# Kernel tuning notes

Measured on AMD Instinct MI355X. Metric: run time of the kernel, lower is better.

## Reference

```python
import jax, jax.numpy as jnp
import numpy as np

D_MODEL = 1024
KEY_MODEL = 1024
D_K = 64
D_V = 64
N_HEAD = 8
PROJ = N_HEAD * D_V  # 512


def setup_inputs() -> dict:
    key = jax.random.key(0)
    ks = jax.random.split(key, 9)
    N, M = 8192, 8192
    s = 0.02
    return {
        "q": jax.random.normal(ks[0], (N, D_MODEL), jnp.float32),
        "k": jax.random.normal(ks[1], (M, KEY_MODEL), jnp.float32),
        "v": jax.random.normal(ks[2], (M, D_MODEL), jnp.float32),
        "Wq": jax.random.normal(ks[3], (D_MODEL, PROJ), jnp.float32) * s,
        "bq": jnp.zeros((PROJ,), jnp.float32),
        "Wk": jax.random.normal(ks[4], (KEY_MODEL, PROJ), jnp.float32) * s,
        "bk": jnp.zeros((PROJ,), jnp.float32),
        "Wv": jax.random.normal(ks[5], (D_MODEL, PROJ), jnp.float32) * s,
        "bv": jnp.zeros((PROJ,), jnp.float32),
    }


def reference(q, k, v, Wq, bq, Wk, bk, Wv, bv):
    # Linear projections (torch nn.Linear: x @ W^T + b; here W stored as [in,out])
    qp = q @ Wq + bq                      # [N, PROJ]
    kp = k @ Wk + bk                      # [M, PROJ]
    vp = v @ Wv + bv                      # [M, PROJ]
    # Note: original scales by d_k (NOT sqrt(d_k)); dropout is identity at eval.
    scores = (qp @ kp.T) / D_K            # [N, M]
    attn = jax.nn.softmax(scores, axis=-1)
    return attn @ vp                      # [N, PROJ]
```

## Files before the change

### kernel.cpp

```cpp
#include <hip/hip_runtime.h>
#include <hip/hip_bf16.h>
#include <stdint.h>
#include <stddef.h>

typedef unsigned short u16;
typedef short bf16x8 __attribute__((ext_vector_type(8)));
typedef short bf16x4 __attribute__((ext_vector_type(4)));
typedef float floatx4 __attribute__((ext_vector_type(4)));

#define N_ROWS 8192
#define D_MODEL 1024
#define PROJ 512
#define MHALF 4096
#define SCALE_LOG2E_DK 0.022542110013890054f

#define VMCNT_WAIT(n) asm volatile("s_waitcnt vmcnt(" #n ")" ::: "memory")

#if __has_builtin(__builtin_amdgcn_exp2f)
#define EXP2(x) __builtin_amdgcn_exp2f(x)
#else
#define EXP2(x) exp2f(x)
#endif

__device__ __forceinline__ float bf2f(u16 u) {
    union { unsigned int i; float f; } x; x.i = ((unsigned int)u) << 16; return x.f;
}
__device__ __forceinline__ u16 f2bf(float f) {
    __hip_bfloat16 h = __float2bfloat16(f);
    return *reinterpret_cast<u16*>(&h);
}

__device__ __forceinline__ void gload_lds16(u16* lds_base, const u16* g) {
    __builtin_amdgcn_global_load_lds(
        (const __attribute__((address_space(1))) void*)g,
        (__attribute__((address_space(3))) void*)lds_base,
        16, 0, 0);
}

__device__ __forceinline__ void stage128x32(u16* lds, const u16* src, int stride,
                                            int wv, int ln) {
    const int rr = ln >> 2;
    const int cc = (ln & 3) << 3;
#pragma unroll
    for (int i = 0; i < 2; ++i) {
        const int rb = i * 64 + wv * 16;
        gload_lds16(lds + rb * 32, src + (size_t)(rb + rr) * stride + cc);
    }
}

__global__ void transpose_w_kernel(const float* __restrict__ in, u16* __restrict__ out,
                                   int R, int C) {
    __shared__ u16 tile[32][33];
    int r = blockIdx.y * 32 + threadIdx.y;
    int c = blockIdx.x * 32 + threadIdx.x;
    tile[threadIdx.y][threadIdx.x] = f2bf(in[(size_t)r * C + c]);
    __syncthreads();
    int ro = blockIdx.x * 32 + threadIdx.y;
    int co = blockIdx.y * 32 + threadIdx.x;
    out[(size_t)ro * R + co] = tile[threadIdx.x][threadIdx.y];
}

__global__ void transpose_kernel(const u16* __restrict__ in, u16* __restrict__ out,
                                 int R, int C) {
    __shared__ u16 tile[32][33];
    int r = blockIdx.y * 32 + threadIdx.y;
    int c = blockIdx.x * 32 + threadIdx.x;
    tile[threadIdx.y][threadIdx.x] = in[(size_t)r * C + c];
    __syncthreads();
    int ro = blockIdx.x * 32 + threadIdx.y;
    int co = blockIdx.y * 32 + threadIdx.x;
    int cp = (co & ~63) | (((co & 15) << 2) + ((co >> 4) & 3));
    out[(size_t)ro * R + cp] = tile[threadIdx.x][threadIdx.y];
}

__global__ __launch_bounds__(256) void convert_bf16_kernel(
    const float* __restrict__ q, const float* __restrict__ k, const float* __restrict__ v,
    u16* __restrict__ qb, u16* __restrict__ kb, u16* __restrict__ vb)
{
    const float* in = (blockIdx.y == 0) ? q : (blockIdx.y == 1) ? k : v;
    u16* out        = (blockIdx.y == 0) ? qb : (blockIdx.y == 1) ? kb : vb;
    size_t i = ((size_t)blockIdx.x * 256 + threadIdx.x) * 8;
    float4 a = *(const float4*)(in + i);
    float4 b = *(const float4*)(in + i + 4);
    bf16x8 o;
    o[0] = (short)f2bf(a.x); o[1] = (short)f2bf(a.y);
    o[2] = (short)f2bf(a.z); o[3] = (short)f2bf(a.w);
    o[4] = (short)f2bf(b.x); o[5] = (short)f2bf(b.y);
    o[6] = (short)f2bf(b.z); o[7] = (short)f2bf(b.w);
    *(bf16x8*)(out + i) = o;
}

__global__ __launch_bounds__(256) void proj_kernel(
    const u16* __restrict__ qb, const u16* __restrict__ kb, const u16* __restrict__ vb,
    const u16* __restrict__ WqT, const u16* __restrict__ WkT, const u16* __restrict__ WvT,
    const float* __restrict__ bq, const float* __restrict__ bk, const float* __restrict__ bv,
    u16* __restrict__ qp, u16* __restrict__ kp, u16* __restrict__ vp)
{
    const int z = blockIdx.z;
    const u16* A      = (z == 0) ? qb  : (z == 1) ? kb  : vb;
    const u16* WT     = (z == 0) ? WqT : (z == 1) ? WkT : WvT;
    const float* bias = (z == 0) ? bq  : (z == 1) ? bk  : bv;
    u16* C            = (z == 0) ? qp  : (z == 1) ? kp  : vp;

    const int m0 = blockIdx.x * 128;
    const int n0 = blockIdx.y * 128;
    __shared__ __align__(16) u16 smem[2 * 128 * 32];
    u16* As = smem;
    u16* Bs = smem + 128 * 32;

    const int t = threadIdx.x;
    const int wv = t >> 6, ln = t & 63;
    const int q16 = ln >> 4, l16 = ln & 15;
    const int wm = (wv & 1) * 64, wn = (wv >> 1) * 64;

    floatx4 acc[4][4] = {};

    for (int k0 = 0; k0 < D_MODEL; k0 += 32) {
        __syncthreads();
        stage128x32(As, A  + (size_t)m0 * D_MODEL + k0, D_MODEL, wv, ln);
        stage128x32(Bs, WT + (size_t)n0 * D_MODEL + k0, D_MODEL, wv, ln);
        __syncthreads();

        bf16x8 af[4], bfr[4];
#pragma unroll
        for (int mi = 0; mi < 4; ++mi)
            af[mi] = *(const bf16x8*)(As + (wm + mi * 16 + l16) * 32 + q16 * 8);
#pragma unroll
        for (int ni = 0; ni < 4; ++ni)
            bfr[ni] = *(const bf16x8*)(Bs + (wn + ni * 16 + l16) * 32 + q16 * 8);
#pragma unroll
        for (int mi = 0; mi < 4; ++mi)
#pragma unroll
            for (int ni = 0; ni < 4; ++ni)
                acc[mi][ni] = __builtin_amdgcn_mfma_f32_16x16x32_bf16(
                    af[mi], bfr[ni], acc[mi][ni], 0, 0, 0);
    }

#pragma unroll
    for (int ni = 0; ni < 4; ++ni) {
        int col = n0 + wn + ni * 16 + l16;
        float bv_ = bias[col];
#pragma unroll
        for (int mi = 0; mi < 4; ++mi)
#pragma unroll
            for (int rr = 0; rr < 4; ++rr) {
                int row = m0 + wm + mi * 16 + q16 * 4 + rr;
                C[(size_t)row * PROJ + col] = f2bf(acc[mi][ni][rr] + bv_);
            }
    }
}

__global__ void zero_l_kernel(float* __restrict__ l) {
    l[blockIdx.x * 256 + threadIdx.x] = 0.f;
}

__global__ __launch_bounds__(256) void score_kernel(
    const u16* __restrict__ qp, const u16* __restrict__ kph,
    u16* __restrict__ P, float* __restrict__ l)
{
    const int m0 = blockIdx.x * 128;
    const int n0 = blockIdx.y * 128;
    __shared__ __align__(16) u16 smem[2 * 128 * 32];
    u16* As = smem;
    u16* Bs = smem + 128 * 32;

    const int t = threadIdx.x;
    const int wv = t >> 6, ln = t & 63;
    const int q16 = ln >> 4, l16 = ln & 15;
    const int wm = (wv & 1) * 64, wn = (wv >> 1) * 64;

    floatx4 acc[4][4] = {};

    for (int k0 = 0; k0 < PROJ; k0 += 32) {
        __syncthreads();
        stage128x32(As, qp  + (size_t)m0 * PROJ + k0, PROJ, wv, ln);
        stage128x32(Bs, kph + (size_t)n0 * PROJ + k0, PROJ, wv, ln);
        __syncthreads();

        bf16x8 af[4], bfr[4];
#pragma unroll
        for (int mi = 0; mi < 4; ++mi)
            af[mi] = *(const bf16x8*)(As + (wm + mi * 16 + l16) * 32 + q16 * 8);
#pragma unroll
        for (int ni = 0; ni < 4; ++ni)
            bfr[ni] = *(const bf16x8*)(Bs + (wn + ni * 16 + l16) * 32 + q16 * 8);
#pragma unroll
        for (int mi = 0; mi < 4; ++mi)
#pragma unroll
            for (int ni = 0; ni < 4; ++ni)
                acc[mi][ni] = __builtin_amdgcn_mfma_f32_16x16x32_bf16(
                    af[mi], bfr[ni], acc[mi][ni], 0, 0, 0);
    }

#pragma unroll
    for (int mi = 0; mi < 4; ++mi)
#pragma unroll
        for (int rr = 0; rr < 4; ++rr) {
            int row = m0 + wm + mi * 16 + q16 * 4 + rr;
            u16* Prow = P + (size_t)row * MHALF + n0 + wn;
            float tot = 0.f;
            bf16x4 pk;
#pragma unroll
            for (int ni = 0; ni < 4; ++ni) {
                float x = acc[mi][ni][rr] * SCALE_LOG2E_DK;
                x = fminf(fmaxf(x, -30.f), 30.f);
                float p = EXP2(x);
                tot += p;
                pk[ni] = (short)f2bf(p);
            }
            *(bf16x4*)(Prow + l16 * 4) = pk;
#pragma unroll
            for (int m = 1; m < 16; m <<= 1)
                tot += __shfl_xor(tot, m, 64);
            if (l16 == 0)
                atomicAdd(&l[row], tot);
        }
}

__global__ __launch_bounds__(256) void pv_kernel(
    const u16* __restrict__ P, const u16* __restrict__ vpTh,
    float* __restrict__ Ofull, u16* __restrict__ Opart, int accum)
{
    const int m0 = blockIdx.x * 128;
    const int n0 = blockIdx.y * 128;
    const int kg = blockIdx.z;
    const int kbase = kg * 2048;
    __shared__ __align__(16) u16 smem[4 * 8192];

    const int t = threadIdx.x;
    const int wv = t >> 6, ln = t & 63;
    const int q16 = ln >> 4, l16 = ln & 15;
    const int wm = (wv & 1) * 64, wn = (wv >> 1) * 64;

    const u16* Abase = P    + (size_t)m0 * MHALF  + kbase;
    const u16* Bbase = vpTh + (size_t)n0 * N_ROWS + kbase;

    floatx4 acc[4][4] = {};

    auto STAGE = [&](int ti) {
        u16* buf = smem + (ti & 3) * 8192;
        stage128x32(buf,        Abase + ti * 32, MHALF,  wv, ln);
        stage128x32(buf + 4096, Bbase + ti * 32, N_ROWS, wv, ln);
    };
    auto COMPUTE = [&](int ti) {
        const u16* As = smem + (ti & 3) * 8192;
        const u16* Bs = As + 4096;
        bf16x8 af[4], bfr[4];
#pragma unroll
        for (int mi = 0; mi < 4; ++mi)
            af[mi] = *(const bf16x8*)(As + (wm + mi * 16 + l16) * 32 + q16 * 8);
#pragma unroll
        for (int ni = 0; ni < 4; ++ni)
            bfr[ni] = *(const bf16x8*)(Bs + (wn + ni * 16 + l16) * 32 + q16 * 8);
#pragma unroll
        for (int mi = 0; mi < 4; ++mi)
#pragma unroll
            for (int ni = 0; ni < 4; ++ni)
                acc[mi][ni] = __builtin_amdgcn_mfma_f32_16x16x32_bf16(
                    af[mi], bfr[ni], acc[mi][ni], 0, 0, 0);
    };

    const int NT = 2048 / 32;
    STAGE(0); STAGE(1); STAGE(2);

    for (int ti = 0; ti < NT - 2; ++ti) {
        VMCNT_WAIT(8);
        __builtin_amdgcn_sched_barrier(0);
        __builtin_amdgcn_s_barrier();
        __builtin_amdgcn_sched_barrier(0);
        if (ti + 3 < NT) STAGE(ti + 3);
        COMPUTE(ti);
    }
    VMCNT_WAIT(4);
    __builtin_amdgcn_sched_barrier(0);
    __builtin_amdgcn_s_barrier();
    __builtin_amdgcn_sched_barrier(0);
    COMPUTE(NT - 2);
    VMCNT_WAIT(0);
    __builtin_amdgcn_sched_barrier(0);
    __builtin_amdgcn_s_barrier();
    __builtin_amdgcn_sched_barrier(0);
    COMPUTE(NT - 1);

#pragma unroll
    for (int ni = 0; ni < 4; ++ni) {
        int col = n0 + wn + ni * 16 + l16;
#pragma unroll
        for (int mi = 0; mi < 4; ++mi)
#pragma unroll
            for (int rr = 0; rr < 4; ++rr) {
                int row = m0 + wm + mi * 16 + q16 * 4 + rr;
                size_t o = (size_t)row * PROJ + col;
                float v = acc[mi][ni][rr];
                if (kg == 0) {
                    if (accum) v += Ofull[o];
                    Ofull[o] = v;
                } else {
                    if (accum) v += bf2f(Opart[o]);
                    Opart[o] = f2bf(v);
                }
            }
    }
}

__global__ void scale_kernel(float* __restrict__ out, const u16* __restrict__ Opart,
                             const float* __restrict__ l)
{
    int idx = blockIdx.x * 256 + threadIdx.x;
    int row = idx >> 9;
    out[idx] = (out[idx] + bf2f(Opart[idx])) / l[row];
}

extern "C" void kernel_launch(void* const* d_in, const int* in_sizes, int n_in,
                              void* d_out, int out_size, void* d_ws, size_t ws_size,
                              hipStream_t stream)
{
    (void)in_sizes; (void)n_in; (void)out_size;
    if (ws_size < ((size_t)101 << 20)) return;

    const float* q  = (const float*)d_in[0];
    const float* k  = (const float*)d_in[1];
    const float* v  = (const float*)d_in[2];
    const float* Wq = (const float*)d_in[3];
    const float* bq = (const float*)d_in[4];
    const float* Wk = (const float*)d_in[5];
    const float* bk = (const float*)d_in[6];
    const float* Wv = (const float*)d_in[7];
    const float* bv = (const float*)d_in[8];

    char* ws = (char*)d_ws;
    u16* qp    = (u16*)(ws);
    u16* kp    = (u16*)(ws + ((size_t)8  << 20));
    u16* vp    = (u16*)(ws + ((size_t)16 << 20));
    u16* vpT   = (u16*)(ws + ((size_t)24 << 20));
    u16* WqT   = (u16*)(ws + ((size_t)32 << 20));
    u16* WkT   = (u16*)(ws + ((size_t)33 << 20));
    u16* WvT   = (u16*)(ws + ((size_t)34 << 20));
    float* l   = (float*)(ws + ((size_t)35 << 20));
    u16* P     = (u16*)(ws + ((size_t)36 << 20));
    u16* qb    = (u16*)(ws + ((size_t)36 << 20));
    u16* kb    = (u16*)(ws + ((size_t)52 << 20));
    u16* vb    = (u16*)(ws + ((size_t)68 << 20));
    u16* Opart = vp;
    float* Ofull = (float*)d_out;

    dim3 tb(32, 32);
    transpose_w_kernel<<<dim3(16, 32), tb, 0, stream>>>(Wq, WqT, 1024, 512);
    transpose_w_kernel<<<dim3(16, 32), tb, 0, stream>>>(Wk, WkT, 1024, 512);
    transpose_w_kernel<<<dim3(16, 32), tb, 0, stream>>>(Wv, WvT, 1024, 512);

    convert_bf16_kernel<<<dim3(4096, 3), 256, 0, stream>>>(q, k, v, qb, kb, vb);

    proj_kernel<<<dim3(64, 4, 3), 256, 0, stream>>>(qb, kb, vb, WqT, WkT, WvT,
                                                    bq, bk, bv, qp, kp, vp);

    transpose_kernel<<<dim3(16, 256), tb, 0, stream>>>(vp, vpT, 8192, 512);

    zero_l_kernel<<<32, 256, 0, stream>>>(l);

    score_kernel<<<dim3(64, 32), 256, 0, stream>>>(qp, kp, P, l);
    pv_kernel<<<dim3(64, 4, 2), 256, 0, stream>>>(P, vpT, Ofull, Opart, 0);
    score_kernel<<<dim3(64, 32), 256, 0, stream>>>(qp, kp + (size_t)MHALF * PROJ, P, l);
    pv_kernel<<<dim3(64, 4, 2), 256, 0, stream>>>(P, vpT + MHALF, Ofull, Opart, 1);

    scale_kernel<<<16384, 256, 0, stream>>>(Ofull, Opart, l);
}
```

Measured before the change: 396.0 us.

## Halve N tile to 64 and double grid for proj and pv kernels

Shrinks the output tile of the projection and PV GEMMs from 128x128 to 128x64, which doubles the number of workgroups so more CUs have work on the 256-CU device. It also swizzles the block-to-tile mapping across XCDs for better L2 locality. The projection kernel moves from a single-buffered, two-barrier loop to the same 4-stage global_load_lds pipeline used in PV. The trade-off is more re-reading of the A operand and lower MFMA arithmetic intensity per block.

```diff
diff --git a/kernel.cpp b/kernel.cpp
--- a/kernel.cpp
+++ b/kernel.cpp
@@ -46,6 +46,14 @@
         const int rb = i * 64 + wv * 16;
         gload_lds16(lds + rb * 32, src + (size_t)(rb + rr) * stride + cc);
     }
+}
+
+__device__ __forceinline__ void stage64x32(u16* lds, const u16* src, int stride,
+                                           int wv, int ln) {
+    const int rr = ln >> 2;
+    const int cc = (ln & 3) << 3;
+    const int rb = wv * 16;
+    gload_lds16(lds + rb * 32, src + (size_t)(rb + rr) * stride + cc);
 }
 
 __global__ void transpose_w_kernel(const float* __restrict__ in, u16* __restrict__ out,
@@ -96,48 +104,75 @@
     const float* __restrict__ bq, const float* __restrict__ bk, const float* __restrict__ bv,
     u16* __restrict__ qp, u16* __restrict__ kp, u16* __restrict__ vp)
 {
-    const int z = blockIdx.z;
+    int orig = blockIdx.x + 64 * (blockIdx.y + 8 * blockIdx.z);
+    int logical = (orig & 7) * 192 + (orig >> 3);
+    const int m0 = (logical & 63) * 128;
+    const int n0 = ((logical >> 6) & 7) * 64;
+    const int z  = logical >> 9;
+
     const u16* A      = (z == 0) ? qb  : (z == 1) ? kb  : vb;
     const u16* WT     = (z == 0) ? WqT : (z == 1) ? WkT : WvT;
     const float* bias = (z == 0) ? bq  : (z == 1) ? bk  : bv;
     u16* C            = (z == 0) ? qp  : (z == 1) ? kp  : vp;
 
-    const int m0 = blockIdx.x * 128;
-    const int n0 = blockIdx.y * 128;
-    __shared__ __align__(16) u16 smem[2 * 128 * 32];
-    u16* As = smem;
-    u16* Bs = smem + 128 * 32;
+    __shared__ __align__(16) u16 smem[4 * 6144];
 
     const int t = threadIdx.x;
     const int wv = t >> 6, ln = t & 63;
     const int q16 = ln >> 4, l16 = ln & 15;
-    const int wm = (wv & 1) * 64, wn = (wv >> 1) * 64;
-
-    floatx4 acc[4][4] = {};
-
-    for (int k0 = 0; k0 < D_MODEL; k0 += 32) {
-        __syncthreads();
-        stage128x32(As, A  + (size_t)m0 * D_MODEL + k0, D_MODEL, wv, ln);
-        stage128x32(Bs, WT + (size_t)n0 * D_MODEL + k0, D_MODEL, wv, ln);
-        __syncthreads();
-
-        bf16x8 af[4], bfr[4];
+    const int wm = (wv & 1) * 64, wn = (wv >> 1) * 32;
+
+    const u16* Abase = A  + (size_t)m0 * D_MODEL;
+    const u16* Bbase = WT + (size_t)n0 * D_MODEL;
+
+    floatx4 acc[4][2] = {};
+
+    auto STAGE = [&](int ti) {
+        u16* buf = smem + (ti & 3) * 6144;
+        stage128x32(buf,        Abase + ti * 32, D_MODEL, wv, ln);
+        stage64x32 (buf + 4096, Bbase + ti * 32, D_MODEL, wv, ln);
+    };
+    auto COMPUTE = [&](int ti) {
+        const u16* As = smem + (ti & 3) * 6144;
+        const u16* Bs = As + 4096;
+        bf16x8 af[4], bfr[2];
 #pragma unroll
         for (int mi = 0; mi < 4; ++mi)
             af[mi] = *(const bf16x8*)(As + (wm + mi * 16 + l16) * 32 + q16 * 8);
 #pragma unroll
-        for (int ni = 0; ni < 4; ++ni)
+        for (int ni = 0; ni < 2; ++ni)
             bfr[ni] = *(const bf16x8*)(Bs + (wn + ni * 16 + l16) * 32 + q16 * 8);
 #pragma unroll
         for (int mi = 0; mi < 4; ++mi)
 #pragma unroll
-            for (int ni = 0; ni < 4; ++ni)
+            for (int ni = 0; ni < 2; ++ni)
                 acc[mi][ni] = __builtin_amdgcn_mfma_f32_16x16x32_bf16(
                     af[mi], bfr[ni], acc[mi][ni], 0, 0, 0);
-    }
-
-#pragma unroll
-    for (int ni = 0; ni < 4; ++ni) {
+    };
+
+    const int NT = D_MODEL / 32;
+    STAGE(0); STAGE(1); STAGE(2);
+    for (int ti = 0; ti < NT - 2; ++ti) {
+        VMCNT_WAIT(6);
+        __builtin_amdgcn_sched_barrier(0);
+        __builtin_amdgcn_s_barrier();
+        __builtin_amdgcn_sched_barrier(0);
+        if (ti + 3 < NT) STAGE(ti + 3);
+        COMPUTE(ti);
+    }
+    VMCNT_WAIT(3);
+    __builtin_amdgcn_sched_barrier(0);
+    __builtin_amdgcn_s_barrier();
+    __builtin_amdgcn_sched_barrier(0);
+    COMPUTE(NT - 2);
+    VMCNT_WAIT(0);
+    __builtin_amdgcn_sched_barrier(0);
+    __builtin_amdgcn_s_barrier();
+    __builtin_amdgcn_sched_barrier(0);
+    COMPUTE(NT - 1);
+
+#pragma unroll
+    for (int ni = 0; ni < 2; ++ni) {
         int col = n0 + wn + ni * 16 + l16;
         float bv_ = bias[col];
 #pragma unroll
@@ -221,41 +256,43 @@
     const u16* __restrict__ P, const u16* __restrict__ vpTh,
     float* __restrict__ Ofull, u16* __restrict__ Opart, int accum)
 {
-    const int m0 = blockIdx.x * 128;
-    const int n0 = blockIdx.y * 128;
-    const int kg = blockIdx.z;
+    int orig = blockIdx.x + 64 * (blockIdx.y + 8 * blockIdx.z);
+    int logical = (orig & 7) * 128 + (orig >> 3);
+    const int m0 = (logical & 63) * 128;
+    const int n0 = ((logical >> 6) & 7) * 64;
+    const int kg = logical >> 9;
     const int kbase = kg * 2048;
-    __shared__ __align__(16) u16 smem[4 * 8192];
+    __shared__ __align__(16) u16 smem[4 * 6144];
 
     const int t = threadIdx.x;
     const int wv = t >> 6, ln = t & 63;
     const int q16 = ln >> 4, l16 = ln & 15;
-    const int wm = (wv & 1) * 64, wn = (wv >> 1) * 64;
+    const int wm = (wv & 1) * 64, wn = (wv >> 1) * 32;
 
     const u16* Abase = P    + (size_t)m0 * MHALF  + kbase;
     const u16* Bbase = vpTh + (size_t)n0 * N_ROWS + kbase;
 
-    floatx4 acc[4][4] = {};
+    floatx4 acc[4][2] = {};
 
     auto STAGE = [&](int ti) {
-        u16* buf = smem + (ti & 3) * 8192;
+        u16* buf = smem + (ti & 3) * 6144;
         stage128x32(buf,        Abase + ti * 32, MHALF,  wv, ln);
-        stage128x32(buf + 4096, Bbase + ti * 32, N_ROWS, wv, ln);
+        stage64x32 (buf + 4096, Bbase + ti * 32, N_ROWS, wv, ln);
     };
     auto COMPUTE = [&](int ti) {
-        const u16* As = smem + (ti & 3) * 8192;
+        const u16* As = smem + (ti & 3) * 6144;
         const u16* Bs = As + 4096;
-        bf16x8 af[4], bfr[4];
+        bf16x8 af[4], bfr[2];
 #pragma unroll
         for (int mi = 0; mi < 4; ++mi)
             af[mi] = *(const bf16x8*)(As + (wm + mi * 16 + l16) * 32 + q16 * 8);
 #pragma unroll
-        for (int ni = 0; ni < 4; ++ni)
+        for (int ni = 0; ni < 2; ++ni)
             bfr[ni] = *(const bf16x8*)(Bs + (wn + ni * 16 + l16) * 32 + q16 * 8);
 #pragma unroll
         for (int mi = 0; mi < 4; ++mi)
 #pragma unroll
-            for (int ni = 0; ni < 4; ++ni)
+            for (int ni = 0; ni < 2; ++ni)
                 acc[mi][ni] = __builtin_amdgcn_mfma_f32_16x16x32_bf16(
                     af[mi], bfr[ni], acc[mi][ni], 0, 0, 0);
     };
@@ -264,14 +301,14 @@
     STAGE(0); STAGE(1); STAGE(2);
 
     for (int ti = 0; ti < NT - 2; ++ti) {
-        VMCNT_WAIT(8);
+        VMCNT_WAIT(6);
         __builtin_amdgcn_sched_barrier(0);
         __builtin_amdgcn_s_barrier();
         __builtin_amdgcn_sched_barrier(0);
         if (ti + 3 < NT) STAGE(ti + 3);
         COMPUTE(ti);
     }
-    VMCNT_WAIT(4);
+    VMCNT_WAIT(3);
     __builtin_amdgcn_sched_barrier(0);
     __builtin_amdgcn_s_barrier();
     __builtin_amdgcn_sched_barrier(0);
@@ -283,7 +320,7 @@
     COMPUTE(NT - 1);
 
 #pragma unroll
-    for (int ni = 0; ni < 4; ++ni) {
+    for (int ni = 0; ni < 2; ++ni) {
         int col = n0 + wn + ni * 16 + l16;
 #pragma unroll
         for (int mi = 0; mi < 4; ++mi)
@@ -351,7 +388,7 @@
 
     convert_bf16_kernel<<<dim3(4096, 3), 256, 0, stream>>>(q, k, v, qb, kb, vb);
 
-    proj_kernel<<<dim3(64, 4, 3), 256, 0, stream>>>(qb, kb, vb, WqT, WkT, WvT,
+    proj_kernel<<<dim3(64, 8, 3), 256, 0, stream>>>(qb, kb, vb, WqT, WkT, WvT,
                                                     bq, bk, bv, qp, kp, vp);
 
     transpose_kernel<<<dim3(16, 256), tb, 0, stream>>>(vp, vpT, 8192, 512);
@@ -359,9 +396,9 @@
     zero_l_kernel<<<32, 256, 0, stream>>>(l);
 
     score_kernel<<<dim3(64, 32), 256, 0, stream>>>(qp, kp, P, l);
-    pv_kernel<<<dim3(64, 4, 2), 256, 0, stream>>>(P, vpT, Ofull, Opart, 0);
+    pv_kernel<<<dim3(64, 8, 2), 256, 0, stream>>>(P, vpT, Ofull, Opart, 0);
     score_kernel<<<dim3(64, 32), 256, 0, stream>>>(qp, kp + (size_t)MHALF * PROJ, P, l);
-    pv_kernel<<<dim3(64, 4, 2), 256, 0, stream>>>(P, vpT + MHALF, Ofull, Opart, 1);
+    pv_kernel<<<dim3(64, 8, 2), 256, 0, stream>>>(P, vpT + MHALF, Ofull, Opart, 1);
 
     scale_kernel<<<16384, 256, 0, stream>>>(Ofull, Opart, l);
 }
```

Measured after the change: 501.5 us. +26.6%, slower.

## Enlarge score kernel tiles to 256x256 with 4-stage async LDS pipeline

Applied to the files above, without the earlier changes.

The score GEMM now uses 256x256 tiles with 512 threads (8 waves, each computing 128x64), which roughly halves global traffic per FLOP. The single-buffered load/sync loop becomes a 4-buffer ring, with three stages prefetched through global_load_lds and vmcnt-based waits, so loads overlap MFMA work and fewer barriers are needed. The costs are 128KB of LDS per block and larger accumulator register pressure. Occupancy drops, and launch_bounds(512,2) may not be reachable with that LDS size.

```diff
diff --git a/kernel.cpp b/kernel.cpp
--- a/kernel.cpp
+++ b/kernel.cpp
@@ -44,6 +44,17 @@
 #pragma unroll
     for (int i = 0; i < 2; ++i) {
         const int rb = i * 64 + wv * 16;
+        gload_lds16(lds + rb * 32, src + (size_t)(rb + rr) * stride + cc);
+    }
+}
+
+__device__ __forceinline__ void stage256x32w(u16* lds, const u16* src, int stride,
+                                             int w, int ln) {
+    const int rr = ln >> 2;
+    const int cc = (ln & 3) << 3;
+#pragma unroll
+    for (int i = 0; i < 2; ++i) {
+        const int rb = i * 128 + w * 16;
         gload_lds16(lds + rb * 32, src + (size_t)(rb + rr) * stride + cc);
     }
 }
@@ -154,50 +165,76 @@
     l[blockIdx.x * 256 + threadIdx.x] = 0.f;
 }
 
-__global__ __launch_bounds__(256) void score_kernel(
+__global__ __launch_bounds__(512, 2) void score_kernel(
     const u16* __restrict__ qp, const u16* __restrict__ kph,
     u16* __restrict__ P, float* __restrict__ l)
 {
-    const int m0 = blockIdx.x * 128;
-    const int n0 = blockIdx.y * 128;
-    __shared__ __align__(16) u16 smem[2 * 128 * 32];
-    u16* As = smem;
-    u16* Bs = smem + 128 * 32;
+    const int m0 = blockIdx.x * 256;
+    const int n0 = blockIdx.y * 256;
+    __shared__ __align__(16) u16 smem[4 * 16384];
 
     const int t = threadIdx.x;
-    const int wv = t >> 6, ln = t & 63;
+    const int w = t >> 6, ln = t & 63;
     const int q16 = ln >> 4, l16 = ln & 15;
-    const int wm = (wv & 1) * 64, wn = (wv >> 1) * 64;
-
-    floatx4 acc[4][4] = {};
-
-    for (int k0 = 0; k0 < PROJ; k0 += 32) {
-        __syncthreads();
-        stage128x32(As, qp  + (size_t)m0 * PROJ + k0, PROJ, wv, ln);
-        stage128x32(Bs, kph + (size_t)n0 * PROJ + k0, PROJ, wv, ln);
-        __syncthreads();
-
-        bf16x8 af[4], bfr[4];
-#pragma unroll
-        for (int mi = 0; mi < 4; ++mi)
-            af[mi] = *(const bf16x8*)(As + (wm + mi * 16 + l16) * 32 + q16 * 8);
+    const int wm2 = w >> 2, wn4 = w & 3;
+    const int wrow = wm2 * 128, wcol = wn4 * 64;
+
+    const u16* Abase = qp  + (size_t)m0 * PROJ;
+    const u16* Bbase = kph + (size_t)n0 * PROJ;
+
+    floatx4 acc[8][4] = {};
+
+    auto STAGE = [&](int ti) {
+        u16* buf = smem + (ti & 3) * 16384;
+        stage256x32w(buf,        Abase + ti * 32, PROJ, w, ln);
+        stage256x32w(buf + 8192, Bbase + ti * 32, PROJ, w, ln);
+    };
+    auto COMPUTE = [&](int ti) {
+        const u16* As = smem + (ti & 3) * 16384;
+        const u16* Bs = As + 8192;
+        bf16x8 af[8], bfr[4];
+#pragma unroll
+        for (int mi = 0; mi < 8; ++mi)
+            af[mi] = *(const bf16x8*)(As + (wrow + mi * 16 + l16) * 32 + q16 * 8);
 #pragma unroll
         for (int ni = 0; ni < 4; ++ni)
-            bfr[ni] = *(const bf16x8*)(Bs + (wn + ni * 16 + l16) * 32 + q16 * 8);
-#pragma unroll
-        for (int mi = 0; mi < 4; ++mi)
+            bfr[ni] = *(const bf16x8*)(Bs + (wcol + ni * 16 + l16) * 32 + q16 * 8);
+#pragma unroll
+        for (int mi = 0; mi < 8; ++mi)
 #pragma unroll
             for (int ni = 0; ni < 4; ++ni)
                 acc[mi][ni] = __builtin_amdgcn_mfma_f32_16x16x32_bf16(
                     af[mi], bfr[ni], acc[mi][ni], 0, 0, 0);
-    }
-
-#pragma unroll
-    for (int mi = 0; mi < 4; ++mi)
+    };
+
+    const int NT = PROJ / 32;
+    STAGE(0); STAGE(1); STAGE(2);
+
+    for (int ti = 0; ti < NT - 2; ++ti) {
+        VMCNT_WAIT(8);
+        __builtin_amdgcn_sched_barrier(0);
+        __builtin_amdgcn_s_barrier();
+        __builtin_amdgcn_sched_barrier(0);
+        if (ti + 3 < NT) STAGE(ti + 3);
+        COMPUTE(ti);
+    }
+    VMCNT_WAIT(4);
+    __builtin_amdgcn_sched_barrier(0);
+    __builtin_amdgcn_s_barrier();
+    __builtin_amdgcn_sched_barrier(0);
+    COMPUTE(NT - 2);
+    VMCNT_WAIT(0);
+    __builtin_amdgcn_sched_barrier(0);
+    __builtin_amdgcn_s_barrier();
+    __builtin_amdgcn_sched_barrier(0);
+    COMPUTE(NT - 1);
+
+#pragma unroll
+    for (int mi = 0; mi < 8; ++mi)
 #pragma unroll
         for (int rr = 0; rr < 4; ++rr) {
-            int row = m0 + wm + mi * 16 + q16 * 4 + rr;
-            u16* Prow = P + (size_t)row * MHALF + n0 + wn;
+            int row = m0 + wrow + mi * 16 + q16 * 4 + rr;
+            u16* Prow = P + (size_t)row * MHALF + n0 + wcol;
             float tot = 0.f;
             bf16x4 pk;
 #pragma unroll
@@ -358,9 +395,9 @@
 
     zero_l_kernel<<<32, 256, 0, stream>>>(l);
 
-    score_kernel<<<dim3(64, 32), 256, 0, stream>>>(qp, kp, P, l);
+    score_kernel<<<dim3(32, 16), 512, 0, stream>>>(qp, kp, P, l);
     pv_kernel<<<dim3(64, 4, 2), 256, 0, stream>>>(P, vpT, Ofull, Opart, 0);
-    score_kernel<<<dim3(64, 32), 256, 0, stream>>>(qp, kp + (size_t)MHALF * PROJ, P, l);
+    score_kernel<<<dim3(32, 16), 512, 0, stream>>>(qp, kp + (size_t)MHALF * PROJ, P, l);
     pv_kernel<<<dim3(64, 4, 2), 256, 0, stream>>>(P, vpT + MHALF, Ofull, Opart, 1);
 
     scale_kernel<<<16384, 256, 0, stream>>>(Ofull, Opart, l);
```

After: 394.2 us. Within noise of the previous version (-0.5%).
